# Performance work log

Hardware: AMD Instinct MI355X
Metric: run time of the kernel (lower is better)

The kernel has to match this reference:

```python
import jax, jax.numpy as jnp
import numpy as np
import math

B, L, N = 8, 2048, 512
H = 16                                  # router hidden_dim
C = min(16, max(2, int(math.sqrt(N))))  # num_centers = 16
D = 64                                  # d_core
STATIC_TOPK = max(32, int(math.sqrt(N) * 2))  # 45


def setup_inputs() -> dict:
    key = jax.random.key(0)
    ks = jax.random.split(key, 32)
    r = lambda i, shape, s=0.05: jax.random.normal(ks[i], shape, jnp.float32) * s
    return dict(
        x=jax.random.normal(ks[0], (B, L, N), jnp.float32),
        var_embed=r(1, (1, N, H), 0.1),
        temp_w=r(2, (2, H)), temp_b=jnp.zeros((H,), jnp.float32),
        q_w=r(3, (2 * H, H)), q_b=jnp.zeros((H,), jnp.float32),
        k_w=r(4, (2 * H, H)), k_b=jnp.zeros((H,), jnp.float32),
        imp_w=r(5, (2 * H, 1)), imp_b=jnp.zeros((1,), jnp.float32),
        cluster_score=r(6, (N, C), 1.0),
        varproj_w=r(7, (C, D)), varproj_b=jnp.zeros((D,), jnp.float32),
        cp1_w=r(8, (D, D)), cp1_b=jnp.zeros((D,), jnp.float32),
        cp2_w=r(9, (D, D)), cp2_b=jnp.zeros((D,), jnp.float32),
        cg_w=r(10, (N, C * D)), cg_b=jnp.zeros((C * D,), jnp.float32),
        gate_w=r(11, (2 * N, N)), gate_b=jnp.zeros((N,), jnp.float32),
        fus_w=r(12, (N, N)), fus_b=jnp.zeros((N,), jnp.float32),
        ln_g=jnp.ones((N,), jnp.float32), ln_b=jnp.zeros((N,), jnp.float32),
    )


def _build_static_mask(x):
    # torch no_grad block: std over batch dim, unbiased (ddof=1)
    xs = jax.lax.stop_gradient(x)
    x_avg = xs.mean(axis=0)                       # [L, N]
    x_std = jnp.std(xs, axis=0, ddof=1) + 1e-5    # [L, N]
    normed = x_avg / x_std
    sim = normed.T @ normed                       # [N, N]
    sim = sim.at[jnp.diag_indices(N)].set(-1e9)
    _, idx = jax.lax.top_k(sim, STATIC_TOPK)      # [N, STATIC_TOPK]
    return jnp.zeros((N, N), bool).at[jnp.arange(N)[:, None], idx].set(True)


def reference(x, var_embed, temp_w, temp_b, q_w, q_b, k_w, k_b, imp_w, imp_b,
              cluster_score, varproj_w, varproj_b, cp1_w, cp1_b, cp2_w, cp2_b,
              cg_w, cg_b, gate_w, gate_b, fus_w, fus_b, ln_g, ln_b):
    mask = _build_static_mask(x)                  # [N, N] bool

    # ---- SparseVariableRouter ----
    x_var = x.transpose(0, 2, 1)                  # [B, N, L]
    mean = x_var.mean(-1, keepdims=True)
    std = jnp.sqrt(jnp.var(x_var, -1, ddof=1, keepdims=True) + 1e-5)
    time_emb = jnp.concatenate([mean, std], -1) @ temp_w + temp_b   # [B, N, H]
    static_emb = jnp.broadcast_to(var_embed, (x.shape[0], N, H))
    var_fused = jnp.concatenate([static_emb, time_emb], -1)         # [B, N, 2H]
    importance = jax.nn.sigmoid(var_fused @ imp_w + imp_b)[..., 0][:, None, :]  # [B,1,N]
    Q = var_fused @ q_w + q_b
    K = var_fused @ k_w + k_b
    sim = jnp.einsum('bnh,bmh->bnm', Q, K) / math.sqrt(H)
    sim = jnp.where(mask[None], sim, -1e9)
    attn = jax.nn.softmax(sim, axis=-1)
    routed = jnp.einsum('bnm,bml->bnl', attn, x_var).transpose(0, 2, 1)  # [B, L, N]
    ring_out = importance * routed + (1.0 - importance) * x

    # ---- multi-center mixing ----
    summary = x.mean(1)                                        # [B, N]
    center_tokens = (summary @ cg_w + cg_b).reshape(-1, C, D)  # [B, C, D]
    cw = jax.nn.softmax(cluster_score, axis=-1)                # [N, C]
    x_center = jnp.einsum('bln,nc->blc', x, cw) @ varproj_w + varproj_b  # [B, L, D]
    cu = center_tokens[:, None, :, :] + x_center[:, :, None, :]          # [B, L, C, D]
    cu = jax.nn.gelu(cu @ cp1_w + cp1_b, approximate=False) @ cp2_w + cp2_b
    center_to_var = jnp.einsum('blcd,nc->bln', cu, cw)         # [B, L, N]

    # ---- gated fusion + layernorm ----
    gate = jax.nn.sigmoid(jnp.concatenate([ring_out, center_to_var], -1) @ gate_w + gate_b)
    fused = gate * ring_out + (1.0 - gate) * center_to_var
    fused = fused @ fus_w + fus_b
    h = fused + x
    mu = h.mean(-1, keepdims=True)
    var = jnp.var(h, -1, keepdims=True)            # biased, as torch LayerNorm
    out = (h - mu) / jnp.sqrt(var + 1e-5) * ln_g + ln_b
    return out
```

## Files before the change

### kernel.cpp

```cpp
#include <hip/hip_runtime.h>

#define B_ 8
#define L_ 2048
#define N_ 512
#define H_ 16
#define C_ 16
#define D_ 64
#define TK_ 45
#define KS_ 16

typedef __attribute__((ext_vector_type(8))) short bf16x8;
typedef __attribute__((ext_vector_type(4))) float f32x4;

__device__ __forceinline__ float sigmoidf_(float v) { return 1.f / (1.f + expf(-v)); }

__device__ __forceinline__ short f2bf(float f) {
  union { float f; unsigned u; } v; v.f = f;
  unsigned r = (v.u + 0x7fffu + ((v.u >> 16) & 1u)) >> 16;
  return (short)r;
}
__device__ __forceinline__ float bf2f(short s) {
  union { unsigned u; float f; } v; v.u = ((unsigned)(unsigned short)s) << 16;
  return v.f;
}
__device__ __forceinline__ void gload16(const void* g, void* l) {
  __builtin_amdgcn_global_load_lds((const __attribute__((address_space(1))) unsigned int*)g,
                                   (__attribute__((address_space(3))) unsigned int*)l, 16, 0, 0);
}

__global__ __launch_bounds__(256) void k_pre(const float* __restrict__ x,
                                             const float* __restrict__ var_embed,
                                             const float* __restrict__ temp_w,
                                             const float* __restrict__ temp_b,
                                             const float* __restrict__ q_w,
                                             const float* __restrict__ q_b,
                                             const float* __restrict__ k_w,
                                             const float* __restrict__ k_b,
                                             const float* __restrict__ imp_w,
                                             const float* __restrict__ imp_b,
                                             const float* __restrict__ cs,
                                             const float* __restrict__ cp2_w,
                                             const float* __restrict__ cp2_b,
                                             const float* __restrict__ vp_b,
                                             const float* __restrict__ vp_w,
                                             const float* __restrict__ cp1_w,
                                             float* __restrict__ normed,
                                             float* __restrict__ psum,
                                             float* __restrict__ psq,
                                             short* __restrict__ xbf,
                                             float* __restrict__ veq,
                                             float* __restrict__ vek,
                                             float* __restrict__ abc,
                                             float* __restrict__ vei,
                                             float* __restrict__ cw,
                                             float* __restrict__ misc) {
  int blk = blockIdx.x, t = threadIdx.x;
  if (blk < 4096) {
    int i = blk * 256 + t;
    float s = 0.f, ss = 0.f;
#pragma unroll
    for (int b = 0; b < B_; ++b) {
      float v = x[b * (L_ * N_) + i];
      s += v; ss += v * v;
    }
    float mean = s * (1.f / B_);
    float var  = fmaxf((ss - s * mean) * (1.f / (B_ - 1)), 0.f);
    normed[i] = mean / (sqrtf(var) + 1e-5f);
  } else if (blk < 4608) {
    int bx = blk - 4096;
    int b  = bx >> 6;
    int ch = bx & 63;
    size_t base = ((size_t)b * L_ + ch * 32) * N_;
    const float* xp = x + base;
    short* xq = xbf + base;
#pragma unroll
    for (int u = 0; u < 2; ++u) {
      int n = t + u * 256;
      float s = 0.f, ss = 0.f;
#pragma unroll 8
      for (int r = 0; r < 32; ++r) {
        float v = xp[r * N_ + n];
        s += v; ss += v * v;
        xq[r * N_ + n] = f2bf(v);
      }
      psum[(b * 64 + ch) * N_ + n] = s;
      psq [(b * 64 + ch) * N_ + n] = ss;
    }
  } else if (blk < 4640) {
    int gid = (blk - 4608) * 256 + t;
    int n = gid >> 4, h = gid & 15;
    float aq = 0.f, ak = 0.f;
#pragma unroll
    for (int i = 0; i < 16; ++i) {
      float ve = var_embed[n * 16 + i];
      aq += ve * q_w[i * 16 + h];
      ak += ve * k_w[i * 16 + h];
    }
    veq[gid] = aq;
    vek[gid] = ak;
  } else if (blk == 4640) {
    if (t < 16) {
      int h = t;
      float Aq = 0.f, Bq = 0.f, Cq = 0.f, Ak = 0.f, Bk = 0.f, Ck = 0.f;
#pragma unroll
      for (int j = 0; j < 16; ++j) {
        float qw = q_w[(16 + j) * 16 + h];
        float kw = k_w[(16 + j) * 16 + h];
        Aq += temp_w[j] * qw; Bq += temp_w[16 + j] * qw; Cq += temp_b[j] * qw;
        Ak += temp_w[j] * kw; Bk += temp_w[16 + j] * kw; Ck += temp_b[j] * kw;
      }
      abc[h]      = Aq; abc[16 + h] = Bq; abc[32 + h] = Cq + q_b[h];
      abc[48 + h] = Ak; abc[64 + h] = Bk; abc[80 + h] = Ck + k_b[h];
    } else if (t == 16) {
      float aI = 0.f, bI = 0.f, cI = 0.f;
#pragma unroll
      for (int j = 0; j < 16; ++j) {
        float iw = imp_w[16 + j];
        aI += temp_w[j] * iw; bI += temp_w[16 + j] * iw; cI += temp_b[j] * iw;
      }
      abc[96] = aI; abc[97] = bI; abc[98] = cI + imp_b[0];
    }
  } else if (blk < 4643) {
    int n = (blk - 4641) * 256 + t;
    float a = 0.f;
#pragma unroll
    for (int i = 0; i < 16; ++i)
      a += var_embed[n * 16 + i] * imp_w[i];
    vei[n] = a;
  } else {
#pragma unroll
    for (int u = 0; u < 2; ++u) {
      int n = t + u * 256;
      float v[16], mx = -3e38f;
#pragma unroll
      for (int c = 0; c < 16; ++c) { v[c] = cs[n * 16 + c]; mx = fmaxf(mx, v[c]); }
      float s = 0.f;
#pragma unroll
      for (int c = 0; c < 16; ++c) { v[c] = expf(v[c] - mx); s += v[c]; }
      float inv = 1.f / s;
#pragma unroll
      for (int c = 0; c < 16; ++c) cw[n * 16 + c] = v[c] * inv;
    }
    if (t < 64) {
      float a = 0.f;
#pragma unroll 8
      for (int d = 0; d < 64; ++d) a += cp2_w[t * 64 + d];
      misc[t] = a;
      float vb = 0.f;
#pragma unroll 8
      for (int e = 0; e < 64; ++e) vb += vp_b[e] * cp1_w[e * 64 + t];
      misc[80 + t] = vb;
    }
    if (t == 0) {
      float bsum = 0.f;
      for (int d = 0; d < 64; ++d) bsum += cp2_b[d];
      misc[64] = bsum;
    }
#pragma unroll
    for (int u = 0; u < 4; ++u) {
      int i = t + u * 256;
      int c = i >> 6, d = i & 63;
      float a = 0.f;
#pragma unroll 8
      for (int e = 0; e < 64; ++e) a += vp_w[c * 64 + e] * cp1_w[e * 64 + d];
      misc[96 + i] = a;
    }
  }
}

__global__ __launch_bounds__(256) void k_sim(const float* __restrict__ nrm,
                                             float* __restrict__ simP) {
  __shared__ float As[32 * 64];
  __shared__ float Bs[32 * 64];
  int bx = blockIdx.x;
  int ks = bx >> 6, tile = bx & 63;
  int bi = tile & 7, bj = tile >> 3;
  int t = threadIdx.x, tx = t & 15, ty = t >> 4;
  float acc[4][4] = {};
  int k0 = ks * (L_ / KS_);
  for (int kt = 0; kt < (L_ / KS_) / 32; ++kt) {
    for (int e = t; e < 2048; e += 256) {
      int kk = e >> 6, i = e & 63;
      int krow = k0 + kt * 32 + kk;
      As[e] = nrm[krow * N_ + bi * 64 + i];
      Bs[e] = nrm[krow * N_ + bj * 64 + i];
    }
    __syncthreads();
#pragma unroll
    for (int kk = 0; kk < 32; ++kk) {
      float4 a = *(const float4*)(As + kk * 64 + ty * 4);
      float4 b = *(const float4*)(Bs + kk * 64 + tx * 4);
      float av[4] = {a.x, a.y, a.z, a.w};
      float bv[4] = {b.x, b.y, b.z, b.w};
#pragma unroll
      for (int i = 0; i < 4; ++i)
#pragma unroll
        for (int j = 0; j < 4; ++j)
          acc[i][j] += av[i] * bv[j];
    }
    __syncthreads();
  }
  float* outp = simP + (size_t)ks * (N_ * N_);
#pragma unroll
  for (int i = 0; i < 4; ++i) {
    int row = bi * 64 + ty * 4 + i;
    float4 o = {acc[i][0], acc[i][1], acc[i][2], acc[i][3]};
    *(float4*)(outp + row * N_ + bj * 64 + tx * 4) = o;
  }
}

__global__ __launch_bounds__(256) void k_simred(const float* __restrict__ simP,
                                                float* __restrict__ sim) {
  int gid = blockIdx.x * 256 + threadIdx.x;
  float4 s = {0.f, 0.f, 0.f, 0.f};
#pragma unroll
  for (int ksi = 0; ksi < KS_; ++ksi) {
    float4 p = *(const float4*)(simP + (size_t)ksi * (N_ * N_) + gid * 4);
    s.x += p.x; s.y += p.y; s.z += p.z; s.w += p.w;
  }
  *(float4*)(sim + gid * 4) = s;
}

__global__ __launch_bounds__(256) void k_tf(
    const float* __restrict__ sim, int* __restrict__ idx_t,
    const float* __restrict__ psum, const float* __restrict__ psq,
    const float* __restrict__ veq, const float* __restrict__ vek,
    const float* __restrict__ abc, const float* __restrict__ vei,
    float* __restrict__ Q, float* __restrict__ Kv,
    float* __restrict__ imp, float* __restrict__ summary) {
  int t = threadIdx.x;
  if (blockIdx.x < 128) {
    int lane = t & 63, wv = t >> 6;
    int n = blockIdx.x * 4 + wv;
    unsigned sv[8];
#pragma unroll
    for (int u = 0; u < 8; ++u) {
      int idx = u * 64 + lane;
      float f = (idx == n) ? -3e38f : sim[n * N_ + idx];
      unsigned xb = __float_as_uint(f);
      sv[u] = (xb & 0x80000000u) ? ~xb : (xb | 0x80000000u);
    }
    unsigned thr = 0u;
#pragma unroll
    for (int b = 31; b >= 0; --b) {
      unsigned cand = thr | (1u << b);
      int cnt = 0;
#pragma unroll
      for (int u = 0; u < 8; ++u)
        cnt += __popcll(__ballot(sv[u] >= cand));
      if (cnt >= TK_) thr = cand;
    }
    int cgt = 0;
#pragma unroll
    for (int u = 0; u < 8; ++u)
      cgt += __popcll(__ballot(sv[u] > thr));
    int need = TK_ - cgt;
    unsigned long long lt_mask = (lane == 0) ? 0ull : (~0ull >> (64 - lane));
    int written = 0, tie_seen = 0;
#pragma unroll
    for (int u = 0; u < 8; ++u) {
      bool gt = sv[u] > thr;
      bool eq = sv[u] == thr;
      unsigned long long me = __ballot(eq);
      bool sel = gt || (eq && (tie_seen + __popcll(me & lt_mask)) < need);
      unsigned long long ms = __ballot(sel);
      int pos = written + __popcll(ms & lt_mask);
      if (sel) idx_t[pos * N_ + n] = u * 64 + lane;
      written += __popcll(ms);
      tie_seen += __popcll(me);
    }
    return;
  }
  int gid = (blockIdx.x - 128) * 256 + t;
  int b = gid >> 9, n = gid & 511;
  float s = 0.f, ss = 0.f;
#pragma unroll 8
  for (int c = 0; c < 64; ++c) {
    s  += psum[(b * 64 + c) * N_ + n];
    ss += psq [(b * 64 + c) * N_ + n];
  }
  float mean = s * (1.f / L_);
  float var  = fmaxf((ss - s * mean) * (1.f / (L_ - 1)), 0.f);
  float stdv = sqrtf(var + 1e-5f);
  summary[b * N_ + n] = mean;
#pragma unroll
  for (int h = 0; h < 16; ++h) {
    Q[(b * N_ + n) * 16 + h]  = veq[n * 16 + h] + mean * abc[h]      + stdv * abc[16 + h] + abc[32 + h];
    Kv[(b * N_ + n) * 16 + h] = vek[n * 16 + h] + mean * abc[48 + h] + stdv * abc[64 + h] + abc[80 + h];
  }
  imp[b * N_ + n] = sigmoidf_(vei[n] + mean * abc[96] + stdv * abc[97] + abc[98]);
}

__global__ __launch_bounds__(256) void k_wprep(const float* __restrict__ gate_w,
                                               const float* __restrict__ fus_w,
                                               const float* __restrict__ cw,
                                               const float* __restrict__ misc,
                                               const float* __restrict__ summ,
                                               const float* __restrict__ cg_w,
                                               const float* __restrict__ cg_b,
                                               short* __restrict__ wt_gate,
                                               short* __restrict__ wt_fus,
                                               short* __restrict__ w2t,
                                               short* __restrict__ cwb,
                                               float* __restrict__ ctP) {
  __shared__ float tile[32][33];
  __shared__ float ssum[8][64];
  int blk = blockIdx.x, t = threadIdx.x;
  if (blk < 512) {
    const float* W = (blk < 256) ? gate_w : fus_w;
    short* Wt = (blk < 256) ? wt_gate : wt_fus;
    int ldd = (blk < 256) ? 1024 : 512;
    int b2 = blk & 255;
    int bk = b2 >> 4, bn = b2 & 15;
    int c = t & 31, r = t >> 5;
    for (int rr = r; rr < 32; rr += 8)
      tile[rr][c] = W[(size_t)(bk * 32 + rr) * 512 + bn * 32 + c];
    __syncthreads();
    for (int rr = r; rr < 32; rr += 8)
      Wt[(size_t)(bn * 32 + rr) * ldd + bk * 32 + c] = f2bf(tile[c][rr]);
  } else if (blk < 544) {
    int gid = (blk - 512) * 256 + t;
    int c = gid >> 9, n = gid & 511;
    float a = 0.f;
    for (int m = 0; m < 512; ++m)
      a += cw[m * 16 + c] * gate_w[(size_t)(512 + m) * 512 + n];
    wt_gate[(size_t)n * 1024 + 512 + c] = f2bf(a);
    wt_gate[(size_t)n * 1024 + 528 + c] = 0;
  } else if (blk < 672) {
    int gid = (blk - 544) * 256 + t;
    int d = gid >> 9, m = gid & 511;
    float a = 0.f;
#pragma unroll
    for (int c = 0; c < 16; ++c)
      a += cw[m * 16 + c] * misc[96 + c * 64 + d];
    w2t[d * 512 + m] = f2bf(a);
  } else if (blk < 736) {
    int gid = (blk - 672) * 256 + t;
    int n = gid >> 5, kk = gid & 31;
    cwb[gid] = (kk < 16) ? f2bf(cw[n * 16 + kk]) : (short)0;
  } else {
    int bx = blk - 736;
    int oc = bx & 31;
    int nc = bx >> 5;
    int n0 = nc * 64;
    for (int e = t; e < 512; e += 256)
      ssum[e >> 6][e & 63] = summ[(e >> 6) * 512 + n0 + (e & 63)];
    __syncthreads();
    int b = t >> 5, ol = t & 31;
    int o = oc * 32 + ol;
    float acc = (nc == 0) ? cg_b[o] : 0.f;
#pragma unroll 8
    for (int k = 0; k < 64; ++k)
      acc += ssum[b][k] * cg_w[(size_t)(n0 + k) * 1024 + o];
    ctP[(nc * 8 + b) * 1024 + o] = acc;
  }
}

__global__ __launch_bounds__(256) void k_caxc(const float* __restrict__ ctP,
                                              const float* __restrict__ cp1_w,
                                              const float* __restrict__ cp1_b,
                                              const float* __restrict__ misc,
                                              float* __restrict__ ctp,
                                              const float* __restrict__ Q,
                                              const float* __restrict__ Kv,
                                              const int* __restrict__ idx_t,
                                              short* __restrict__ At,
                                              const short* __restrict__ xbf,
                                              const short* __restrict__ w2t,
                                              float* __restrict__ xcp) {
  __shared__ float cts[256];
  __shared__ short rowbuf[4][512];
  __shared__ __align__(16) short As[2][64 * 32];
  __shared__ __align__(16) short Bs[2][64 * 32];
  int blk = blockIdx.x, t = threadIdx.x;
  if (blk < 32) {
    int row0 = blk * 4;
    int b = row0 >> 4, c0 = row0 & 15;
    {
      int idx = (c0 + (t >> 6)) * 64 + (t & 63);
      float a = 0.f;
#pragma unroll
      for (int p = 0; p < 8; ++p) a += ctP[(p * 8 + b) * 1024 + idx];
      cts[t] = a;
    }
    __syncthreads();
    int lr = t >> 6, d2 = t & 63;
    float a = cp1_b[d2] + misc[80 + d2];
#pragma unroll 8
    for (int d = 0; d < 64; ++d) a += cts[lr * 64 + d] * cp1_w[d * 64 + d2];
    ctp[(row0 + lr) * 64 + d2] = a;
  } else if (blk < 32 + 1024) {
    int w = t >> 6, j = t & 63;
    int bn = (blk - 32) * 4 + w;
    int b = bn >> 9, n = bn & (N_ - 1);
    ((int4*)rowbuf[w])[j] = int4{0, 0, 0, 0};
    float s = -3e38f;
    int m = 0;
    if (j < TK_) {
      m = idx_t[j * N_ + n];
      const float* qp = Q + (b * N_ + n) * H_;
      const float* kp = Kv + (b * N_ + m) * H_;
      float a = 0.f;
#pragma unroll
      for (int h = 0; h < H_; ++h) a += qp[h] * kp[h];
      s = a * 0.25f;
    }
    float mx = s;
#pragma unroll
    for (int o = 32; o > 0; o >>= 1) mx = fmaxf(mx, __shfl_xor(mx, o));
    float e = (j < TK_) ? expf(s - mx) : 0.f;
    float sum = e;
#pragma unroll
    for (int o = 32; o > 0; o >>= 1) sum += __shfl_xor(sum, o);
    __syncthreads();
    if (j < TK_) rowbuf[w][m] = f2bf(e / sum);
    __syncthreads();
    ((int4*)(At + (size_t)bn * 512))[j] = ((int4*)rowbuf[w])[j];
  } else {
    int lane = t & 63, w = t >> 6;
    int lo = lane & 15, hi = lane >> 4;
    int row0 = (blk - 1056) * 64;
    f32x4 acc[4] = {};
    int rA = t >> 2, cA = (t & 3) ^ ((rA >> 1) & 3);
    const short* srcA = xbf + (size_t)(row0 + rA) * 512 + cA * 8;
    const short* srcB = w2t + (size_t)rA * 512 + cA * 8;
    int gl = (lo >> 1) & 3;
    int foff = (lo * 4 + (hi ^ gl)) * 8;
    gload16(srcA, As[0] + t * 8);
    gload16(srcB, Bs[0] + t * 8);
    __syncthreads();
    int cur = 0;
    for (int kt = 0; kt < 16; ++kt) {
      if (kt < 15) {
        gload16(srcA + (kt + 1) * 32, As[cur ^ 1] + t * 8);
        gload16(srcB + (kt + 1) * 32, Bs[cur ^ 1] + t * 8);
      }
      bf16x8 b = *(const bf16x8*)(Bs[cur] + (w * 64) * 8 + foff);
#pragma unroll
      for (int m = 0; m < 4; ++m) {
        bf16x8 a = *(const bf16x8*)(As[cur] + (m * 64) * 8 + foff);
        acc[m] = __builtin_amdgcn_mfma_f32_16x16x32_bf16(a, b, acc[m], 0, 0, 0);
      }
      __syncthreads();
      cur ^= 1;
    }
#pragma unroll
    for (int m = 0; m < 4; ++m)
#pragma unroll
      for (int j = 0; j < 4; ++j) {
        int row = row0 + m * 16 + hi * 4 + j;
        int col = w * 16 + lo;
        xcp[(size_t)row * 64 + col] = acc[m][j];
      }
  }
}

__global__ __launch_bounds__(512) void k_sg(const short* __restrict__ xbf,
                                            const short* __restrict__ At,
                                            const float* __restrict__ imp,
                                            short* __restrict__ abuf,
                                            const float* __restrict__ xcp,
                                            const float* __restrict__ ctp,
                                            const float* __restrict__ misc) {
  __shared__ __align__(16) short As[2][128 * 32];
  __shared__ __align__(16) short Bs[2][128 * 32];
  int blk = blockIdx.x, t = threadIdx.x;
  int lane = t & 63, w = t >> 6;
  if (blk < 512) {
    int lo = lane & 15, hi = lane >> 4;
    int b = blk >> 6;
    int tile = blk & 63;
    int bm = tile >> 2, bn = tile & 3;
    int row0 = b * L_ + bm * 128, n0 = bn * 128;
    int wm = w >> 2, wn = w & 3;
    f32x4 acc[4][2] = {};
    int rs = t >> 2, cs = (t & 3) ^ ((rs >> 1) & 3);
    const short* sA = xbf + (size_t)(row0 + rs) * 512 + cs * 8;
    const short* sB = At + ((size_t)b * N_ + n0 + rs) * 512 + cs * 8;
    int gl = (lo >> 1) & 3;
    int foff = (lo * 4 + (hi ^ gl)) * 8;
    gload16(sA, As[0] + t * 8);
    gload16(sB, Bs[0] + t * 8);
    __syncthreads();
    int cur = 0;
    for (int i = 0; i < 16; ++i) {
      if (i < 15) {
        gload16(sA + (i + 1) * 32, As[cur ^ 1] + t * 8);
        gload16(sB + (i + 1) * 32, Bs[cur ^ 1] + t * 8);
      }
      bf16x8 a[4], bb[2];
#pragma unroll
      for (int m = 0; m < 4; ++m)
        a[m] = *(const bf16x8*)(As[cur] + (wm * 64 + m * 16) * 32 + foff);
#pragma unroll
      for (int n = 0; n < 2; ++n)
        bb[n] = *(const bf16x8*)(Bs[cur] + (wn * 32 + n * 16) * 32 + foff);
#pragma unroll
      for (int m = 0; m < 4; ++m)
#pragma unroll
        for (int n = 0; n < 2; ++n)
          acc[m][n] = __builtin_amdgcn_mfma_f32_16x16x32_bf16(a[m], bb[n], acc[m][n], 0, 0, 0);
      __syncthreads();
      cur ^= 1;
    }
#pragma unroll
    for (int m = 0; m < 4; ++m) {
      int rbase = row0 + wm * 64 + m * 16 + hi * 4;
#pragma unroll
      for (int j = 0; j < 4; ++j) {
        int row = rbase + j;
#pragma unroll
        for (int n = 0; n < 2; ++n) {
          int col = n0 + wn * 32 + n * 16 + lo;
          float iv = imp[b * N_ + col];
          float xv = bf2f(xbf[(size_t)row * 512 + col]);
          abuf[(size_t)row * 1024 + col] = f2bf(iv * acc[m][n][j] + (1.f - iv) * xv);
        }
      }
    }
  } else {
    int row = (blk - 512) * 8 + w;
    int b = row >> 11;
    float v = xcp[(size_t)row * 64 + lane];
    float wgt = misc[lane];
    float bias = misc[64];
    float sval = 0.f;
#pragma unroll
    for (int c = 0; c < 16; ++c) {
      float u = ctp[(b * 16 + c) * 64 + lane] + v;
      float g = 0.5f * u * (1.f + erff(u * 0.70710678118654752f));
      float a = g * wgt;
#pragma unroll
      for (int o = 32; o > 0; o >>= 1) a += __shfl_xor(a, o);
      if (lane == c) sval = a + bias;
    }
    if (lane < 32)
      abuf[(size_t)row * 1024 + 512 + lane] = (lane < 16) ? f2bf(sval) : (short)0;
  }
}

__global__ __launch_bounds__(512) void k_gemm_gate(const short* __restrict__ abuf,
                                                   const short* __restrict__ wt,
                                                   const short* __restrict__ cwb,
                                                   const float* __restrict__ gate_b,
                                                   short* __restrict__ fused_bf) {
  __shared__ __align__(16) short As[2][128 * 32];
  __shared__ __align__(16) short Bs[2][128 * 32];
  int t = threadIdx.x, lane = t & 63, w = t >> 6;
  int lo = lane & 15, hi = lane >> 4;
  int bm = blockIdx.x >> 2, bn = blockIdx.x & 3;
  int row0 = bm * 128, n0 = bn * 128;
  int wm = w >> 2, wn = w & 3;
  f32x4 acc[4][2] = {};
  f32x4 acc2[4][2] = {};
  int rs = t >> 2, cs = (t & 3) ^ ((rs >> 1) & 3);
  const short* sA = abuf + (size_t)(row0 + rs) * 1024 + cs * 8;
  const short* sB = wt + (size_t)(n0 + rs) * 1024 + cs * 8;
  int gl = (lo >> 1) & 3;
  int foff = (lo * 4 + (hi ^ gl)) * 8;
  gload16(sA + 16 * 32, As[0] + t * 8);
  gload16(cwb + (size_t)(n0 + rs) * 32 + cs * 8, Bs[0] + t * 8);
  gload16(sA, As[1] + t * 8);
  gload16(sB, Bs[1] + t * 8);
  __syncthreads();
  {
    bf16x8 a[4], bb[2];
#pragma unroll
    for (int m = 0; m < 4; ++m)
      a[m] = *(const bf16x8*)(As[0] + (wm * 64 + m * 16) * 32 + foff);
#pragma unroll
    for (int n = 0; n < 2; ++n)
      bb[n] = *(const bf16x8*)(Bs[0] + (wn * 32 + n * 16) * 32 + foff);
#pragma unroll
    for (int m = 0; m < 4; ++m)
#pragma unroll
      for (int n = 0; n < 2; ++n)
        acc2[m][n] = __builtin_amdgcn_mfma_f32_16x16x32_bf16(a[m], bb[n], acc2[m][n], 0, 0, 0);
  }
  __syncthreads();
  int cur = 1;
  for (int i = 1; i <= 17; ++i) {
    if (i < 17) {
      gload16(sA + i * 32, As[cur ^ 1] + t * 8);
      gload16(sB + i * 32, Bs[cur ^ 1] + t * 8);
    }
    bf16x8 a[4], bb[2];
#pragma unroll
    for (int m = 0; m < 4; ++m)
      a[m] = *(const bf16x8*)(As[cur] + (wm * 64 + m * 16) * 32 + foff);
#pragma unroll
    for (int n = 0; n < 2; ++n)
      bb[n] = *(const bf16x8*)(Bs[cur] + (wn * 32 + n * 16) * 32 + foff);
#pragma unroll
    for (int m = 0; m < 4; ++m)
#pragma unroll
      for (int n = 0; n < 2; ++n)
        acc[m][n] = __builtin_amdgcn_mfma_f32_16x16x32_bf16(a[m], bb[n], acc[m][n], 0, 0, 0);
    __syncthreads();
    cur ^= 1;
  }
#pragma unroll
  for (int m = 0; m < 4; ++m) {
    int rbase = row0 + wm * 64 + m * 16 + hi * 4;
#pragma unroll
    for (int j = 0; j < 4; ++j) {
      int row = rbase + j;
#pragma unroll
      for (int n = 0; n < 2; ++n) {
        int col = n0 + wn * 32 + n * 16 + lo;
        float g = sigmoidf_(acc[m][n][j] + gate_b[col]);
        float ringv = bf2f(abuf[(size_t)row * 1024 + col]);
        fused_bf[(size_t)row * 512 + col] = f2bf(g * ringv + (1.f - g) * acc2[m][n][j]);
      }
    }
  }
}

__global__ __launch_bounds__(512) void k_gemm_fus(const short* __restrict__ fused_bf,
                                                  const short* __restrict__ wtf,
                                                  const float* __restrict__ x,
                                                  const float* __restrict__ fus_b,
                                                  const float* __restrict__ ln_g,
                                                  const float* __restrict__ ln_b,
                                                  float* __restrict__ out) {
  __shared__ __align__(16) short As[2][64 * 32];
  __shared__ __align__(16) short Bs[2][512 * 32];
  __shared__ float Ssh[8][64], Qsh[8][64];
  __shared__ float mus[64], rss[64];
  int t = threadIdx.x, lane = t & 63, w = t >> 6;
  int lo = lane & 15, hi = lane >> 4;
  int row0 = blockIdx.x * 64;
  f32x4 acc[4][4] = {};
  int pA = w * 64 + lane;
  int rA = pA >> 2, cA = (pA & 3) ^ ((rA >> 1) & 3);
  const short* srcA = fused_bf + (size_t)(row0 + rA) * 512 + cA * 8;
  int rB[4], cB[4];
  const short* srcB[4];
#pragma unroll
  for (int q = 0; q < 4; ++q) {
    int pB = w * 256 + q * 64 + lane;
    rB[q] = pB >> 2; cB[q] = (pB & 3) ^ ((rB[q] >> 1) & 3);
    srcB[q] = wtf + (size_t)rB[q] * 512 + cB[q] * 8;
  }
  int gl = (lo >> 1) & 3;
  int foff = (lo * 4 + (hi ^ gl)) * 8;
  if (w < 4) gload16(srcA, As[0] + pA * 8);
#pragma unroll
  for (int q = 0; q < 4; ++q)
    gload16(srcB[q], Bs[0] + (w * 256 + q * 64) * 8);
  __syncthreads();
  int cur = 0;
  for (int i = 0; i < 16; ++i) {
    if (i < 15) {
      int kt = i + 1;
      if (w < 4) gload16(srcA + kt * 32, As[cur ^ 1] + pA * 8);
#pragma unroll
      for (int q = 0; q < 4; ++q)
        gload16(srcB[q] + kt * 32, Bs[cur ^ 1] + (w * 256 + q * 64) * 8);
    }
    bf16x8 a[4], b[4];
#pragma unroll
    for (int m = 0; m < 4; ++m)
      a[m] = *(const bf16x8*)(As[cur] + (m * 64) * 8 + foff);
#pragma unroll
    for (int n = 0; n < 4; ++n)
      b[n] = *(const bf16x8*)(Bs[cur] + (w * 256 + n * 64) * 8 + foff);
#pragma unroll
    for (int m = 0; m < 4; ++m)
#pragma unroll
      for (int n = 0; n < 4; ++n)
        acc[m][n] = __builtin_amdgcn_mfma_f32_16x16x32_bf16(a[m], b[n], acc[m][n], 0, 0, 0);
    __syncthreads();
    cur ^= 1;
  }
#pragma unroll
  for (int m = 0; m < 4; ++m) {
#pragma unroll
    for (int j = 0; j < 4; ++j) {
      int rl = m * 16 + hi * 4 + j;
      int row = row0 + rl;
      float ps = 0.f, pq = 0.f;
#pragma unroll
      for (int n = 0; n < 4; ++n) {
        int col = w * 64 + n * 16 + lo;
        float h = acc[m][n][j] + fus_b[col] + x[(size_t)row * 512 + col];
        acc[m][n][j] = h;
        ps += h; pq += h * h;
      }
#pragma unroll
      for (int o = 1; o < 16; o <<= 1) {
        ps += __shfl_xor(ps, o);
        pq += __shfl_xor(pq, o);
      }
      if (lo == 0) { Ssh[w][rl] = ps; Qsh[w][rl] = pq; }
    }
  }
  __syncthreads();
  if (t < 64) {
    float s = 0.f, q = 0.f;
#pragma unroll
    for (int ww = 0; ww < 8; ++ww) { s += Ssh[ww][t]; q += Qsh[ww][t]; }
    float mu = s * (1.f / N_);
    float var = q * (1.f / N_) - mu * mu;
    mus[t] = mu;
    rss[t] = rsqrtf(fmaxf(var, 0.f) + 1e-5f);
  }
  __syncthreads();
#pragma unroll
  for (int m = 0; m < 4; ++m) {
#pragma unroll
    for (int j = 0; j < 4; ++j) {
      int rl = m * 16 + hi * 4 + j;
      int row = row0 + rl;
      float mu = mus[rl], rs = rss[rl];
#pragma unroll
      for (int n = 0; n < 4; ++n) {
        int col = w * 64 + n * 16 + lo;
        out[(size_t)row * 512 + col] = (acc[m][n][j] - mu) * rs * ln_g[col] + ln_b[col];
      }
    }
  }
}

extern "C" void kernel_launch(void* const* d_in, const int* in_sizes, int n_in,
                              void* d_out, int out_size, void* d_ws, size_t ws_size,
                              hipStream_t stream) {
  (void)in_sizes; (void)n_in; (void)out_size; (void)ws_size;
  const float* x         = (const float*)d_in[0];
  const float* var_embed = (const float*)d_in[1];
  const float* temp_w    = (const float*)d_in[2];
  const float* temp_b    = (const float*)d_in[3];
  const float* q_w       = (const float*)d_in[4];
  const float* q_b       = (const float*)d_in[5];
  const float* k_w       = (const float*)d_in[6];
  const float* k_b       = (const float*)d_in[7];
  const float* imp_w     = (const float*)d_in[8];
  const float* imp_b     = (const float*)d_in[9];
  const float* cluster   = (const float*)d_in[10];
  const float* vp_w      = (const float*)d_in[11];
  const float* vp_b      = (const float*)d_in[12];
  const float* cp1_w     = (const float*)d_in[13];
  const float* cp1_b     = (const float*)d_in[14];
  const float* cp2_w     = (const float*)d_in[15];
  const float* cp2_b     = (const float*)d_in[16];
  const float* cg_w      = (const float*)d_in[17];
  const float* cg_b      = (const float*)d_in[18];
  const float* gate_w    = (const float*)d_in[19];
  const float* gate_b    = (const float*)d_in[20];
  const float* fus_w     = (const float*)d_in[21];
  const float* fus_b     = (const float*)d_in[22];
  const float* ln_g      = (const float*)d_in[23];
  const float* ln_b      = (const float*)d_in[24];
  float* out = (float*)d_out;
  float* ws  = (float*)d_ws;

  float* normed = ws + 0;
  int*   idx_t  = (int*)(ws + 1310720);
  float* Qb     = ws + 1335296;
  float* Kb     = ws + 1400832;
  float* impb   = ws + 1466368;
  float* summ   = ws + 1470464;
  float* cw     = ws + 1658880;
  float* ctp    = ws + 1675264;
  float* misc   = ws + 1683456;
  short* w2t    = (short*)(ws + 1693696);
  short* cwb    = (short*)(ws + 1710080);
  short* abuf     = (short*)(ws + 1720320);
  short* fused_bf = (short*)(ws + 10108928);
  short* wt_gate  = (short*)(ws + 14303232);
  short* wt_fus   = (short*)(ws + 14565376);
  float* psum     = ws + 14696448;
  float* psq      = ws + 14958592;
  float* ctP      = ws + 15220736;
  short* At       = (short*)(ws + 15286272);
  float* sim      = ws + 16334848;
  float* veq      = ws + 16596992;
  float* vek      = ws + 16605184;
  float* abc      = ws + 16613376;
  float* vei      = ws + 16613504;
  float* simP = (float*)abuf;
  float* xcp  = normed;
  short* xbf  = fused_bf;

  k_pre<<<4644, 256, 0, stream>>>(x, var_embed, temp_w, temp_b, q_w, q_b, k_w, k_b,
                                  imp_w, imp_b, cluster, cp2_w, cp2_b, vp_b, vp_w,
                                  cp1_w, normed, psum, psq, xbf, veq, vek, abc, vei,
                                  cw, misc);
  k_sim<<<64 * KS_, 256, 0, stream>>>(normed, simP);
  k_simred<<<256, 256, 0, stream>>>(simP, sim);
  k_tf<<<144, 256, 0, stream>>>(sim, idx_t, psum, psq, veq, vek, abc, vei,
                                Qb, Kb, impb, summ);
  k_wprep<<<992, 256, 0, stream>>>(gate_w, fus_w, cw, misc, summ, cg_w, cg_b,
                                   wt_gate, wt_fus, w2t, cwb, ctP);
  k_caxc<<<1312, 256, 0, stream>>>(ctP, cp1_w, cp1_b, misc, ctp, Qb, Kb, idx_t,
                                   At, xbf, w2t, xcp);
  k_sg<<<2560, 512, 0, stream>>>(xbf, At, impb, abuf, xcp, ctp, misc);
  k_gemm_gate<<<512, 512, 0, stream>>>(abuf, wt_gate, cwb, gate_b, fused_bf);
  k_gemm_fus<<<256, 512, 0, stream>>>(fused_bf, wt_fus, x, fus_b, ln_g, ln_b, out);
}
```

Before: 191.5 us.

## Fuse batch-stat and per-batch column-sum passes over x into one read

Merges the two k_pre passes over x (batch mean/std for the similarity input, and per-batch column sums with bf16 conversion) into one pass where each block covers 8 rows across all batches. The partial sums grow to 256 chunks per batch, so a second-level reduction is added as extra blocks in k_simred and k_tf reads the reduced values. This removes one full read of the large input at the cost of fewer, larger blocks in k_pre and a serial reduction stage; new workspace offsets extend beyond the previous layout.

```diff
diff --git a/kernel.cpp b/kernel.cpp
--- a/kernel.cpp
+++ b/kernel.cpp
@@ -28,7 +28,7 @@
                                    (__attribute__((address_space(3))) unsigned int*)l, 16, 0, 0);
 }
 
-__global__ __launch_bounds__(256) void k_pre(const float* __restrict__ x,
+__global__ __launch_bounds__(512) void k_pre(const float* __restrict__ x,
                                              const float* __restrict__ var_embed,
                                              const float* __restrict__ temp_w,
                                              const float* __restrict__ temp_b,
@@ -55,39 +55,34 @@
                                              float* __restrict__ cw,
                                              float* __restrict__ misc) {
   int blk = blockIdx.x, t = threadIdx.x;
-  if (blk < 4096) {
-    int i = blk * 256 + t;
-    float s = 0.f, ss = 0.f;
+  if (blk < 256) {
+    int l0 = blk * 8;
+    int n = t;
+    float row_s[8] = {}, row_ss[8] = {};
 #pragma unroll
     for (int b = 0; b < B_; ++b) {
-      float v = x[b * (L_ * N_) + i];
-      s += v; ss += v * v;
-    }
-    float mean = s * (1.f / B_);
-    float var  = fmaxf((ss - s * mean) * (1.f / (B_ - 1)), 0.f);
-    normed[i] = mean / (sqrtf(var) + 1e-5f);
-  } else if (blk < 4608) {
-    int bx = blk - 4096;
-    int b  = bx >> 6;
-    int ch = bx & 63;
-    size_t base = ((size_t)b * L_ + ch * 32) * N_;
-    const float* xp = x + base;
-    short* xq = xbf + base;
-#pragma unroll
-    for (int u = 0; u < 2; ++u) {
-      int n = t + u * 256;
-      float s = 0.f, ss = 0.f;
-#pragma unroll 8
-      for (int r = 0; r < 32; ++r) {
-        float v = xp[r * N_ + n];
-        s += v; ss += v * v;
-        xq[r * N_ + n] = f2bf(v);
-      }
-      psum[(b * 64 + ch) * N_ + n] = s;
-      psq [(b * 64 + ch) * N_ + n] = ss;
-    }
-  } else if (blk < 4640) {
-    int gid = (blk - 4608) * 256 + t;
+      float bs = 0.f, bss = 0.f;
+#pragma unroll
+      for (int r = 0; r < 8; ++r) {
+        float v = x[((size_t)b * L_ + l0 + r) * N_ + n];
+        bs += v; bss += v * v;
+        row_s[r] += v; row_ss[r] += v * v;
+        xbf[((size_t)b * L_ + l0 + r) * N_ + n] = f2bf(v);
+      }
+      psum[((size_t)b * 256 + blk) * N_ + n] = bs;
+      psq [((size_t)b * 256 + blk) * N_ + n] = bss;
+    }
+#pragma unroll
+    for (int r = 0; r < 8; ++r) {
+      float mean = row_s[r] * (1.f / B_);
+      float var  = fmaxf((row_ss[r] - row_s[r] * mean) * (1.f / (B_ - 1)), 0.f);
+      normed[(l0 + r) * N_ + n] = mean / (sqrtf(var) + 1e-5f);
+    }
+    return;
+  }
+  if (t >= 256) return;
+  if (blk < 288) {
+    int gid = (blk - 256) * 256 + t;
     int n = gid >> 4, h = gid & 15;
     float aq = 0.f, ak = 0.f;
 #pragma unroll
@@ -98,7 +93,7 @@
     }
     veq[gid] = aq;
     vek[gid] = ak;
-  } else if (blk == 4640) {
+  } else if (blk == 288) {
     if (t < 16) {
       int h = t;
       float Aq = 0.f, Bq = 0.f, Cq = 0.f, Ak = 0.f, Bk = 0.f, Ck = 0.f;
@@ -120,8 +115,8 @@
       }
       abc[96] = aI; abc[97] = bI; abc[98] = cI + imp_b[0];
     }
-  } else if (blk < 4643) {
-    int n = (blk - 4641) * 256 + t;
+  } else if (blk < 291) {
+    int n = (blk - 289) * 256 + t;
     float a = 0.f;
 #pragma unroll
     for (int i = 0; i < 16; ++i)
@@ -210,20 +205,38 @@
 }
 
 __global__ __launch_bounds__(256) void k_simred(const float* __restrict__ simP,
-                                                float* __restrict__ sim) {
-  int gid = blockIdx.x * 256 + threadIdx.x;
-  float4 s = {0.f, 0.f, 0.f, 0.f};
-#pragma unroll
-  for (int ksi = 0; ksi < KS_; ++ksi) {
-    float4 p = *(const float4*)(simP + (size_t)ksi * (N_ * N_) + gid * 4);
-    s.x += p.x; s.y += p.y; s.z += p.z; s.w += p.w;
-  }
-  *(float4*)(sim + gid * 4) = s;
+                                                float* __restrict__ sim,
+                                                const float* __restrict__ psum,
+                                                const float* __restrict__ psq,
+                                                float* __restrict__ psumR,
+                                                float* __restrict__ psqR) {
+  int t = threadIdx.x;
+  if (blockIdx.x < 256) {
+    int gid = blockIdx.x * 256 + t;
+    float4 s = {0.f, 0.f, 0.f, 0.f};
+#pragma unroll
+    for (int ksi = 0; ksi < KS_; ++ksi) {
+      float4 p = *(const float4*)(simP + (size_t)ksi * (N_ * N_) + gid * 4);
+      s.x += p.x; s.y += p.y; s.z += p.z; s.w += p.w;
+    }
+    *(float4*)(sim + gid * 4) = s;
+    return;
+  }
+  int tid = (blockIdx.x - 256) * 256 + t;
+  const float* src = (tid < 4096) ? psum : psq;
+  float* dst = (tid < 4096) ? psumR : psqR;
+  int id = tid & 4095;
+  int b = id >> 9, n = id & 511;
+  float a = 0.f;
+#pragma unroll 8
+  for (int c = 0; c < 256; ++c)
+    a += src[((size_t)b * 256 + c) * N_ + n];
+  dst[id] = a;
 }
 
 __global__ __launch_bounds__(256) void k_tf(
     const float* __restrict__ sim, int* __restrict__ idx_t,
-    const float* __restrict__ psum, const float* __restrict__ psq,
+    const float* __restrict__ psumR, const float* __restrict__ psqR,
     const float* __restrict__ veq, const float* __restrict__ vek,
     const float* __restrict__ abc, const float* __restrict__ vei,
     float* __restrict__ Q, float* __restrict__ Kv,
@@ -273,12 +286,8 @@
   }
   int gid = (blockIdx.x - 128) * 256 + t;
   int b = gid >> 9, n = gid & 511;
-  float s = 0.f, ss = 0.f;
-#pragma unroll 8
-  for (int c = 0; c < 64; ++c) {
-    s  += psum[(b * 64 + c) * N_ + n];
-    ss += psq [(b * 64 + c) * N_ + n];
-  }
+  float s  = psumR[gid];
+  float ss = psqR[gid];
   float mean = s * (1.f / L_);
   float var  = fmaxf((ss - s * mean) * (1.f / (L_ - 1)), 0.f);
   float stdv = sqrtf(var + 1e-5f);
@@ -769,8 +778,6 @@
   short* fused_bf = (short*)(ws + 10108928);
   short* wt_gate  = (short*)(ws + 14303232);
   short* wt_fus   = (short*)(ws + 14565376);
-  float* psum     = ws + 14696448;
-  float* psq      = ws + 14958592;
   float* ctP      = ws + 15220736;
   short* At       = (short*)(ws + 15286272);
   float* sim      = ws + 16334848;
@@ -778,17 +785,21 @@
   float* vek      = ws + 16605184;
   float* abc      = ws + 16613376;
   float* vei      = ws + 16613504;
+  float* psum     = ws + 17000000;
+  float* psq      = ws + 18100000;
+  float* psumR    = ws + 19200000;
+  float* psqR     = ws + 19210000;
   float* simP = (float*)abuf;
   float* xcp  = normed;
   short* xbf  = fused_bf;
 
-  k_pre<<<4644, 256, 0, stream>>>(x, var_embed, temp_w, temp_b, q_w, q_b, k_w, k_b,
-                                  imp_w, imp_b, cluster, cp2_w, cp2_b, vp_b, vp_w,
-                                  cp1_w, normed, psum, psq, xbf, veq, vek, abc, vei,
-                                  cw, misc);
+  k_pre<<<292, 512, 0, stream>>>(x, var_embed, temp_w, temp_b, q_w, q_b, k_w, k_b,
+                                 imp_w, imp_b, cluster, cp2_w, cp2_b, vp_b, vp_w,
+                                 cp1_w, normed, psum, psq, xbf, veq, vek, abc, vei,
+                                 cw, misc);
   k_sim<<<64 * KS_, 256, 0, stream>>>(normed, simP);
-  k_simred<<<256, 256, 0, stream>>>(simP, sim);
-  k_tf<<<144, 256, 0, stream>>>(sim, idx_t, psum, psq, veq, vek, abc, vei,
+  k_simred<<<288, 256, 0, stream>>>(simP, sim, psum, psq, psumR, psqR);
+  k_tf<<<144, 256, 0, stream>>>(sim, idx_t, psumR, psqR, veq, vek, abc, vei,
                                 Qb, Kb, impb, summ);
   k_wprep<<<992, 256, 0, stream>>>(gate_w, fus_w, cw, misc, summ, cg_w, cg_b,
                                    wt_gate, wt_fus, w2t, cwb, ctP);
```

After: 195.1 us. No clear change (+1.8%).
